# Optimization experiments

Measured on AMD Instinct MI355X. Metric: run time of the kernel, lower is better.

The kernel has to match this reference:

```python
import jax, jax.numpy as jnp
import numpy as np

B, N, C = 4, 4096, 64
K1, K2 = 4, 6
MLP1 = [128, 64, 64]
MLP2 = [128, 64]
EPS = 1e-5


def _sqdist(a, b):
    # a: [B,N,3], b: [B,M,3] -> [B,N,M]
    return (jnp.sum(a * a, -1)[:, :, None] + jnp.sum(b * b, -1)[:, None, :]
            - 2.0 * jnp.einsum('bnc,bmc->bnm', a, b))


def _knn_idx(k, xyz, new_xyz):
    # matches knn_point: topk of -square_distance(new_xyz, xyz)
    _, idx = jax.lax.top_k(-_sqdist(new_xyz, xyz), k)
    return idx  # [B,S,k]


def _gather(points, idx):
    # index_points: points [B,N,C], idx [B,S,K] -> [B,S,K,C]
    return jax.vmap(lambda p, i: p[i])(points, idx)


def _conv_bn_relu(x, w, g, b):
    # 1x1 Conv2d (no bias) + BatchNorm2d (train mode) + ReLU, channels-last
    y = jnp.einsum('bnkc,oc->bnko', x, w)
    m = jnp.mean(y, axis=(0, 1, 2), keepdims=True)
    v = jnp.var(y, axis=(0, 1, 2), keepdims=True)
    return jax.nn.relu((y - m) * jax.lax.rsqrt(v + EPS) * g + b)


def _quat_mul(a, b):
    # Hamilton product, matches mul_q_point ordering
    aw, ax, ay, az = a[..., 0], a[..., 1], a[..., 2], a[..., 3]
    bw, bx, by, bz = b[..., 0], b[..., 1], b[..., 2], b[..., 3]
    return jnp.stack([
        aw * bw - ax * bx - ay * by - az * bz,
        aw * bx + ax * bw + ay * bz - az * by,
        aw * by - ax * bz + ay * bw + az * bx,
        aw * bz + ax * by - ay * bx + az * bw], axis=-1)


def _inv_q(q):
    n2 = jnp.sum(q * q, -1, keepdims=True) + 1e-10
    return jnp.concatenate([q[..., :1], -q[..., 1:]], -1) / n2


def _qrot(q, v):
    # rotate points v [B,M,3] by quaternion q [B,4] via q * (0,v) * q^-1
    vq = jnp.concatenate([jnp.zeros(v.shape[:-1] + (1,), v.dtype), v], -1)
    qb = q[:, None, :]
    return _quat_mul(_quat_mul(qb, vq), _inv_q(q)[:, None, :])[..., 1:]


def setup_inputs() -> dict:
    key = jax.random.key(0)
    ks = jax.random.split(key, 32)

    def rn(i, shape, s=1.0):
        return jax.random.normal(ks[i], shape, jnp.float32) * s

    inp = {
        'pos1': rn(0, (B, N, 3)),
        'pos2': rn(1, (B, N, 3)),
        'feat1': rn(2, (B, N, C)),
        'feat2': rn(3, (B, N, C)),
        'q_coarse': rn(4, (B, 4)),
        't_coarse': rn(5, (B, 3)),
    }
    c1 = [2 * C + 3] + MLP1
    for i in range(len(MLP1)):
        inp['w1_%d' % i] = rn(6 + i, (c1[i + 1], c1[i]), 0.1)
        inp['g1_%d' % i] = jnp.ones((c1[i + 1],), jnp.float32)
        inp['b1_%d' % i] = jnp.zeros((c1[i + 1],), jnp.float32)
    c2 = [MLP1[-1] + C + 3] + MLP2
    for i in range(len(MLP2)):
        inp['w2_%d' % i] = rn(12 + i, (c2[i + 1], c2[i]), 0.1)
        inp['g2_%d' % i] = jnp.ones((c2[i + 1],), jnp.float32)
        inp['b2_%d' % i] = jnp.zeros((c2[i + 1],), jnp.float32)
    inp['wq'] = rn(20, (4, MLP2[-1]), 0.01)
    inp['bq'] = jnp.zeros((4,), jnp.float32)
    inp['wt'] = rn(21, (3, MLP2[-1]), 0.01)
    inp['bt'] = jnp.zeros((3,), jnp.float32)
    return inp


def reference(pos1, pos2, feat1, feat2, q_coarse, t_coarse,
              w1_0, g1_0, b1_0, w1_1, g1_1, b1_1, w1_2, g1_2, b1_2,
              w2_0, g2_0, b2_0, w2_1, g2_1, b2_1, wq, bq, wt, bt):
    # warp pos1 by the coarse pose (q, t)
    pos1_w = _qrot(q_coarse, pos1) + t_coarse[:, None, :]

    # cross-cloud KNN grouping (FlowEmbedding first stage)
    idx2 = _knn_idx(K2, pos2, pos1_w)                      # [B,N,K2]
    xd2 = _gather(pos2, idx2) - pos1_w[:, :, None, :]      # [B,N,K2,3]
    f2g = _gather(feat2, idx2)                             # [B,N,K2,C]
    f1r = jnp.broadcast_to(feat1[:, :, None, :], (B, N, K2, C))
    x = jnp.concatenate([xd2, f2g, f1r], -1)               # [B,N,K2,131]
    for w, g, b in ((w1_0, g1_0, b1_0), (w1_1, g1_1, b1_1), (w1_2, g1_2, b1_2)):
        x = _conv_bn_relu(x, w, g, b)
    fe = jnp.sum(x, axis=2)                                # [B,N,64] sum pool over neighbors

    # self KNN grouping (FlowEmbedding second stage)
    idx1 = _knn_idx(K1, pos1_w, pos1_w)                    # [B,N,K1]
    xd1 = _gather(pos1_w, idx1) - pos1_w[:, :, None, :]
    feg = _gather(fe, idx1)
    f1r2 = jnp.broadcast_to(feat1[:, :, None, :], (B, N, K1, C))
    x = jnp.concatenate([xd1, feg, f1r2], -1)              # [B,N,K1,131]
    for w, g, b in ((w2_0, g2_0, b2_0), (w2_1, g2_1, b2_1)):
        x = _conv_bn_relu(x, w, g, b)
    pooled = jnp.sum(jnp.sum(x, axis=2), axis=1)           # [B,64] sum pool

    # pose delta heads + quaternion composition
    q_det = pooled @ wq.T + bq
    q_det = q_det / (jnp.linalg.norm(q_det, axis=-1, keepdims=True) + 1e-10)
    t_det = pooled @ wt.T + bt
    q_new = _quat_mul(q_det, q_coarse)
    q_new = q_new / (jnp.linalg.norm(q_new, axis=-1, keepdims=True) + 1e-10)
    t_new = _qrot(q_det, t_coarse[:, None, :])[:, 0, :] + t_det
    return jnp.concatenate([q_new, t_new], -1)             # [B,7]
```

## Files before the change

kernel.cpp:

```cpp
#include <hip/hip_runtime.h>
#include <math.h>

#define B_ 4
#define N_ 4096
#define C_ 64
#define K1_ 4
#define K2_ 6
#define EPS_ 1e-5f
#define BN_ (B_ * N_)
#define NCH_ 16
#define CHP_ 256
#define STKD_ 16

typedef __attribute__((ext_vector_type(8))) short bf16x8;
typedef __attribute__((ext_vector_type(4))) float f32x4;
typedef __attribute__((ext_vector_type(2))) float f32x2;

__device__ __forceinline__ unsigned short f2bf(float f) {
  unsigned int u = __float_as_uint(f);
  unsigned int r = (u + 0x7fffu + ((u >> 16) & 1u)) >> 16;
  return (unsigned short)r;
}
__device__ __forceinline__ float bf2f(unsigned short u) {
  return __uint_as_float(((unsigned int)u) << 16);
}

__global__ __launch_bounds__(256) void k_init(
    const float* __restrict__ w1_0, const float* __restrict__ w1_1,
    const float* __restrict__ w1_2, const float* __restrict__ w2_0,
    const float* __restrict__ w2_1, unsigned short* __restrict__ Wf2a,
    unsigned short* __restrict__ Wf1a, unsigned short* __restrict__ Wfe,
    unsigned short* __restrict__ Wf1b, unsigned short* __restrict__ wb1,
    unsigned short* __restrict__ wb2, unsigned short* __restrict__ wb4,
    const float* __restrict__ pos1, const float* __restrict__ pos2,
    const float* __restrict__ qc, const float* __restrict__ tc,
    float* __restrict__ posw, float4* __restrict__ pts4w, float4* __restrict__ pairW,
    float4* __restrict__ pairP) {
  int t = blockIdx.x * 256 + threadIdx.x;
  int m = blockIdx.y;
  if (m < 7) {
    switch (m) {
      case 0:
        if (t < 8192) Wf2a[t] = f2bf(w1_0[(t >> 6) * 131 + 3 + (t & 63)]);
        break;
      case 1:
        if (t < 8192) Wf1a[t] = f2bf(w1_0[(t >> 6) * 131 + 67 + (t & 63)]);
        break;
      case 2:
        if (t < 8192) Wfe[t] = f2bf(w2_0[(t >> 6) * 131 + 3 + (t & 63)]);
        break;
      case 3:
        if (t < 8192) Wf1b[t] = f2bf(w2_0[(t >> 6) * 131 + 67 + (t & 63)]);
        break;
      case 4:
        if (t < 8192) wb1[t] = f2bf(w1_1[t]);
        break;
      case 5:
        if (t < 4096) wb2[t] = f2bf(w1_2[t]);
        break;
      default:
        if (t < 8192) wb4[t] = f2bf(w2_1[t]);
        break;
    }
    return;
  }
  if (t >= BN_) return;
  int b = t / N_;
  float qw = qc[b * 4 + 0], qx = qc[b * 4 + 1], qy = qc[b * 4 + 2], qz = qc[b * 4 + 3];
  float vx = pos1[t * 3 + 0], vy = pos1[t * 3 + 1], vz = pos1[t * 3 + 2];
  float aw = -(qx * vx + qy * vy + qz * vz);
  float ax = qw * vx + qy * vz - qz * vy;
  float ay = qw * vy - qx * vz + qz * vx;
  float az = qw * vz + qx * vy - qy * vx;
  float n2 = qw * qw + qx * qx + qy * qy + qz * qz + 1e-10f;
  float bw = qw / n2, bx = -qx / n2, by = -qy / n2, bz = -qz / n2;
  float rx = aw * bx + ax * bw + ay * bz - az * by;
  float ry = aw * by - ax * bz + ay * bw + az * bx;
  float rz = aw * bz + ax * by - ay * bx + az * bw;
  rx += tc[b * 3 + 0];
  ry += tc[b * 3 + 1];
  rz += tc[b * 3 + 2];
  posw[t * 3 + 0] = rx;
  posw[t * 3 + 1] = ry;
  posw[t * 3 + 2] = rz;
  float rw2 = rx * rx + ry * ry + rz * rz;
  pts4w[t] = make_float4(rx, ry, rz, rw2);
  int p = t >> 1, h = t & 1;
  float* bwp = (float*)&pairW[(size_t)2 * p];
  bwp[0 + h] = rx; bwp[2 + h] = ry; bwp[4 + h] = rz; bwp[6 + h] = rw2;
  float px = pos2[t * 3 + 0], py = pos2[t * 3 + 1], pz = pos2[t * 3 + 2];
  float pw2 = px * px + py * py + pz * pz;
  float* bpp = (float*)&pairP[(size_t)2 * p];
  bpp[0 + h] = px; bpp[2 + h] = py; bpp[4 + h] = pz; bpp[6 + h] = pw2;
}

__device__ __forceinline__ void ins6i(int (&kd)[6], int k) {
  int x = k;
#pragma unroll
  for (int u = 0; u < 6; ++u) {
    int lo = min(kd[u], x);
    x = max(kd[u], x);
    kd[u] = lo;
  }
}

__global__ __launch_bounds__(256) void k_knn2(const float4* __restrict__ pts4w,
                                              const float4* __restrict__ pairW,
                                              const float4* __restrict__ pairP,
                                              int* __restrict__ outK) {
  __shared__ int st[STKD_][256];
  int tid = threadIdx.x;
  int b = blockIdx.z & 3;
  int which = blockIdx.z >> 2;
  const f32x4* __restrict__ PT =
      (const f32x4*)((which ? pairW : pairP) + (size_t)b * N_ + blockIdx.y * CHP_);
  int base = blockIdx.y * CHP_;
  int n = blockIdx.x * 256 + tid;
  float4 qv = pts4w[(size_t)b * N_ + n];
  f32x2 qq2 = (f32x2)(qv.w);
  f32x2 m2x = (f32x2)(-2.f * qv.x);
  f32x2 m2y = (f32x2)(-2.f * qv.y);
  f32x2 m2z = (f32x2)(-2.f * qv.z);
  int kd[6];
#pragma unroll
  for (int t = 0; t < 6; ++t) kd[t] = 0x7fffffff;
  int kbd5 = 0x7fffffff;
  int ptr = 0;
  for (int jj = 0; jj < CHP_; jj += 4) {
    f32x4 e0 = PT[jj + 0];
    f32x4 e1 = PT[jj + 1];
    f32x4 e2 = PT[jj + 2];
    f32x4 e3 = PT[jj + 3];
    f32x2 d01 = __builtin_elementwise_fma(
        m2x, e0.xy,
        __builtin_elementwise_fma(m2y, e0.zw,
                                  __builtin_elementwise_fma(m2z, e1.xy, e1.zw + qq2)));
    f32x2 d23 = __builtin_elementwise_fma(
        m2x, e2.xy,
        __builtin_elementwise_fma(m2y, e2.zw,
                                  __builtin_elementwise_fma(m2z, e3.xy, e3.zw + qq2)));
    int j0 = base + jj;
    int k0 = (int)((__float_as_uint(d01.x) & 0xFFFFF000u) | (unsigned)(j0 + 0));
    int k1 = (int)((__float_as_uint(d01.y) & 0xFFFFF000u) | (unsigned)(j0 + 1));
    int k2 = (int)((__float_as_uint(d23.x) & 0xFFFFF000u) | (unsigned)(j0 + 2));
    int k3 = (int)((__float_as_uint(d23.y) & 0xFFFFF000u) | (unsigned)(j0 + 3));
    st[ptr][tid] = k0;
    ptr += (k0 < kbd5) ? 1 : 0;
    st[ptr][tid] = k1;
    ptr += (k1 < kbd5) ? 1 : 0;
    st[ptr][tid] = k2;
    ptr += (k2 < kbd5) ? 1 : 0;
    st[ptr][tid] = k3;
    ptr += (k3 < kbd5) ? 1 : 0;
    if (__ballot(ptr >= STKD_ - 4)) {
      for (int i = 0; i < ptr; ++i) ins6i(kd, st[i][tid]);
      ptr = 0;
      kbd5 = kd[5];
    }
  }
  for (int i = 0; i < ptr; ++i) ins6i(kd, st[i][tid]);
  size_t ob =
      ((size_t)which * BN_ * NCH_ + (size_t)(b * N_ + n) * NCH_ + blockIdx.y) * 6;
#pragma unroll
  for (int t = 0; t < 6; ++t) outK[ob + t] = kd[t];
}

__global__ __launch_bounds__(64) void k_knn2_merge(const int* __restrict__ inK,
                                                   int* __restrict__ idx2,
                                                   int* __restrict__ idx1) {
  int t = blockIdx.x * 64 + threadIdx.x;
  if (t >= 2 * BN_) return;
  int which = (t >= BN_) ? 1 : 0;
  int qi = t - which * BN_;
  int kd[6];
#pragma unroll
  for (int u = 0; u < 6; ++u) kd[u] = 0x7fffffff;
  size_t ib = ((size_t)which * BN_ + qi) * NCH_ * 6;
  for (int c = 0; c < NCH_ * 6; ++c) ins6i(kd, inK[ib + c]);
  if (which) {
#pragma unroll
    for (int u = 0; u < K1_; ++u) idx1[(size_t)qi * K1_ + u] = kd[u] & 0xFFF;
  } else {
#pragma unroll
    for (int u = 0; u < K2_; ++u) idx2[(size_t)qi * K2_ + u] = kd[u] & 0xFFF;
  }
}

__global__ __launch_bounds__(256) void k_proj(
    const float* __restrict__ s0, const unsigned short* __restrict__ w0,
    float* __restrict__ d0, const float* __restrict__ s1,
    const unsigned short* __restrict__ w1, float* __restrict__ d1,
    const float* __restrict__ s2, const unsigned short* __restrict__ w2,
    float* __restrict__ d2) {
  const float* src;
  const unsigned short* Wb;
  float* dst;
  switch (blockIdx.y) {
    case 0: src = s0; Wb = w0; dst = d0; break;
    case 1: src = s1; Wb = w1; dst = d1; break;
    default: src = s2; Wb = w2; dst = d2; break;
  }
  constexpr int SP = 72;
  __shared__ unsigned short Xs[64 * SP];
  int tid = threadIdx.x;
  int row0 = blockIdx.x * 64;
  for (int e = tid; e < 64 * 16; e += 256) {
    int r = e >> 4, s = e & 15;
    float4 v = *(const float4*)&src[(size_t)(row0 + r) * 64 + s * 4];
    ushort4 o;
    o.x = f2bf(v.x); o.y = f2bf(v.y); o.z = f2bf(v.z); o.w = f2bf(v.w);
    *(ushort4*)&Xs[r * SP + s * 4] = o;
  }
  __syncthreads();
  int l = tid & 63, wv = tid >> 6;
  int lm = l & 15, quad = l >> 4;
  int n0 = wv * 32;
  f32x4 acc[4][2];
#pragma unroll
  for (int rt = 0; rt < 4; ++rt)
#pragma unroll
    for (int ct = 0; ct < 2; ++ct) acc[rt][ct] = (f32x4)(0.f);
#pragma unroll
  for (int k0 = 0; k0 < 64; k0 += 32) {
    bf16x8 a[4], b[2];
#pragma unroll
    for (int rt = 0; rt < 4; ++rt)
      a[rt] = *(const bf16x8*)&Xs[(rt * 16 + lm) * SP + k0 + quad * 8];
#pragma unroll
    for (int ct = 0; ct < 2; ++ct)
      b[ct] = *(const bf16x8*)&Wb[(size_t)(n0 + ct * 16 + lm) * 64 + k0 + quad * 8];
#pragma unroll
    for (int rt = 0; rt < 4; ++rt)
#pragma unroll
      for (int ct = 0; ct < 2; ++ct)
        acc[rt][ct] =
            __builtin_amdgcn_mfma_f32_16x16x32_bf16(a[rt], b[ct], acc[rt][ct], 0, 0, 0);
  }
#pragma unroll
  for (int rt = 0; rt < 4; ++rt)
#pragma unroll
    for (int ct = 0; ct < 2; ++ct)
#pragma unroll
      for (int r = 0; r < 4; ++r) {
        int row = row0 + rt * 16 + quad * 4 + r;
        dst[(size_t)row * 128 + n0 + ct * 16 + lm] = acc[rt][ct][r];
      }
}

template <int KNN>
__global__ __launch_bounds__(256) void k_asm(
    const float* __restrict__ Wfull,
    const float* __restrict__ posP, const float* __restrict__ posw,
    const float* __restrict__ Pj, const float* __restrict__ Pn,
    const int* __restrict__ idx, unsigned short* __restrict__ yout,
    float* __restrict__ statOut) {
  __shared__ float Wx[3][128];
  __shared__ float red[16][128];
  int tid = threadIdx.x;
  if (tid < 128) {
    Wx[0][tid] = Wfull[tid * 131 + 0];
    Wx[1][tid] = Wfull[tid * 131 + 1];
    Wx[2][tid] = Wfull[tid * 131 + 2];
  }
  __syncthreads();
  int cg = tid & 15, rg = tid >> 4;
  int c0 = cg * 8;
  int row0 = blockIdx.x * 128 + rg * 8;
  float wx0[8], wx1[8], wx2[8];
#pragma unroll
  for (int u = 0; u < 8; ++u) {
    wx0[u] = Wx[0][c0 + u];
    wx1[u] = Wx[1][c0 + u];
    wx2[u] = Wx[2][c0 + u];
  }
  float s1[8], s2[8];
#pragma unroll
  for (int u = 0; u < 8; ++u) { s1[u] = 0.f; s2[u] = 0.f; }
#pragma unroll
  for (int i = 0; i < 8; ++i) {
    int row = row0 + i;
    int g = row / KNN;
    int bb = g >> 12;
    int j = idx[row];
    int gj = (bb << 12) + j;
    float xd0 = posP[(size_t)gj * 3 + 0] - posw[(size_t)g * 3 + 0];
    float xd1 = posP[(size_t)gj * 3 + 1] - posw[(size_t)g * 3 + 1];
    float xd2 = posP[(size_t)gj * 3 + 2] - posw[(size_t)g * 3 + 2];
    const float* pj = &Pj[(size_t)gj * 128 + c0];
    const float* pn = &Pn[(size_t)g * 128 + c0];
    float4 a0 = *(const float4*)&pj[0];
    float4 a1 = *(const float4*)&pj[4];
    float4 b0 = *(const float4*)&pn[0];
    float4 b1 = *(const float4*)&pn[4];
    float y[8];
    y[0] = a0.x + b0.x; y[1] = a0.y + b0.y; y[2] = a0.z + b0.z; y[3] = a0.w + b0.w;
    y[4] = a1.x + b1.x; y[5] = a1.y + b1.y; y[6] = a1.z + b1.z; y[7] = a1.w + b1.w;
    ushort4 o0, o1;
    unsigned short ob[8];
#pragma unroll
    for (int u = 0; u < 8; ++u) {
      float v = y[u];
      v = fmaf(xd0, wx0[u], v);
      v = fmaf(xd1, wx1[u], v);
      v = fmaf(xd2, wx2[u], v);
      s1[u] += v;
      s2[u] = fmaf(v, v, s2[u]);
      ob[u] = f2bf(v);
    }
    o0.x = ob[0]; o0.y = ob[1]; o0.z = ob[2]; o0.w = ob[3];
    o1.x = ob[4]; o1.y = ob[5]; o1.z = ob[6]; o1.w = ob[7];
    *(ushort4*)&yout[(size_t)row * 128 + c0] = o0;
    *(ushort4*)&yout[(size_t)row * 128 + c0 + 4] = o1;
  }
  int slot = blockIdx.x & 7;
#pragma unroll
  for (int u = 0; u < 8; ++u) red[rg][c0 + u] = s1[u];
  __syncthreads();
  if (tid < 128) {
    float s = 0.f;
#pragma unroll
    for (int r = 0; r < 16; ++r) s += red[r][tid];
    atomicAdd(&statOut[tid * 8 + slot], s);
  }
  __syncthreads();
#pragma unroll
  for (int u = 0; u < 8; ++u) red[rg][c0 + u] = s2[u];
  __syncthreads();
  if (tid < 128) {
    float s = 0.f;
#pragma unroll
    for (int r = 0; r < 16; ++r) s += red[r][tid];
    atomicAdd(&statOut[128 * 8 + tid * 8 + slot], s);
  }
}

template <int CIN, int COUT, int KP>
__global__ __launch_bounds__(256) void k_layer_mfma(
    const unsigned short* __restrict__ Wb,
    const unsigned short* __restrict__ yprev,
    const float* __restrict__ statPrev, const float* __restrict__ gPrev,
    const float* __restrict__ bPrev, float prevInvM,
    unsigned short* __restrict__ yout,
    float* __restrict__ statOut) {
  constexpr int SP = KP + 8;
  constexpr int CST = COUT + 8;
  constexpr int CT = COUT / 64;
  __shared__ unsigned short Xs[64 * SP];
  __shared__ float scl[CIN];
  __shared__ float shf[CIN];

  int tid = threadIdx.x;
  int row0 = blockIdx.x * 64;

  for (int c = tid; c < CIN; c += 256) {
    float s = 0.f, s2 = 0.f;
#pragma unroll
    for (int u = 0; u < 8; ++u) {
      s += statPrev[c * 8 + u];
      s2 += statPrev[CIN * 8 + c * 8 + u];
    }
    float m = s * prevInvM;
    float v = s2 * prevInvM - m * m;
    float sc = gPrev[c] * rsqrtf(v + EPS_);
    scl[c] = sc;
    shf[c] = bPrev[c] - m * sc;
  }
  __syncthreads();
  constexpr int S4 = KP / 4;
  for (int e = tid; e < 64 * S4; e += 256) {
    int r = e / S4, s = e - r * S4;
    int row = row0 + r;
    ushort4 u = *(const ushort4*)&yprev[(size_t)row * CIN + s * 4];
    ushort4 o;
    o.x = f2bf(fmaxf(fmaf(bf2f(u.x), scl[s * 4 + 0], shf[s * 4 + 0]), 0.f));
    o.y = f2bf(fmaxf(fmaf(bf2f(u.y), scl[s * 4 + 1], shf[s * 4 + 1]), 0.f));
    o.z = f2bf(fmaxf(fmaf(bf2f(u.z), scl[s * 4 + 2], shf[s * 4 + 2]), 0.f));
    o.w = f2bf(fmaxf(fmaf(bf2f(u.w), scl[s * 4 + 3], shf[s * 4 + 3]), 0.f));
    *(ushort4*)&Xs[r * SP + s * 4] = o;
  }
  __syncthreads();

  int l = tid & 63, wv = tid >> 6;
  int lm = l & 15, quad = l >> 4;
  int n0 = wv * (COUT / 4);

  f32x4 acc[4][CT];
#pragma unroll
  for (int rt = 0; rt < 4; ++rt)
#pragma unroll
    for (int ct = 0; ct < CT; ++ct) acc[rt][ct] = (f32x4)(0.f);

#pragma unroll
  for (int k0 = 0; k0 < KP; k0 += 32) {
    bf16x8 a[4], b[CT];
#pragma unroll
    for (int rt = 0; rt < 4; ++rt)
      a[rt] = *(const bf16x8*)&Xs[(rt * 16 + lm) * SP + k0 + quad * 8];
#pragma unroll
    for (int ct = 0; ct < CT; ++ct)
      b[ct] = *(const bf16x8*)&Wb[(size_t)(n0 + ct * 16 + lm) * KP + k0 + quad * 8];
#pragma unroll
    for (int rt = 0; rt < 4; ++rt)
#pragma unroll
      for (int ct = 0; ct < CT; ++ct)
        acc[rt][ct] =
            __builtin_amdgcn_mfma_f32_16x16x32_bf16(a[rt], b[ct], acc[rt][ct], 0, 0, 0);
  }

  int slot = blockIdx.x & 7;
#pragma unroll
  for (int ct = 0; ct < CT; ++ct) {
    float s1 = 0.f, s2 = 0.f;
#pragma unroll
    for (int rt = 0; rt < 4; ++rt)
#pragma unroll
      for (int r = 0; r < 4; ++r) {
        float v = acc[rt][ct][r];
        s1 += v;
        s2 += v * v;
      }
    s1 += __shfl_xor(s1, 16);
    s1 += __shfl_xor(s1, 32);
    s2 += __shfl_xor(s2, 16);
    s2 += __shfl_xor(s2, 32);
    if (quad == 0) {
      int col = n0 + ct * 16 + lm;
      atomicAdd(&statOut[col * 8 + slot], s1);
      atomicAdd(&statOut[COUT * 8 + col * 8 + slot], s2);
    }
  }

  __syncthreads();
  unsigned short* Ys = Xs;
#pragma unroll
  for (int rt = 0; rt < 4; ++rt)
#pragma unroll
    for (int ct = 0; ct < CT; ++ct)
#pragma unroll
      for (int r = 0; r < 4; ++r)
        Ys[(rt * 16 + quad * 4 + r) * CST + n0 + ct * 16 + lm] = f2bf(acc[rt][ct][r]);
  __syncthreads();
  constexpr int S8 = COUT / 8;
  for (int e = tid; e < 64 * S8; e += 256) {
    int r = e / S8, c0 = (e - r * S8) * 8;
    uint4 v = *(const uint4*)&Ys[r * CST + c0];
    *(uint4*)&yout[((size_t)(row0 + r)) * COUT + c0] = v;
  }
}

__global__ __launch_bounds__(256) void k_fe(const unsigned short* __restrict__ y3,
                                            const float* __restrict__ stat,
                                            const float* __restrict__ g,
                                            const float* __restrict__ bb,
                                            float* __restrict__ fe) {
  __shared__ float scl[C_], shf[C_];
  if (threadIdx.x < C_) {
    int c = threadIdx.x;
    float s = 0.f, s2 = 0.f;
#pragma unroll
    for (int u = 0; u < 8; ++u) {
      s += stat[c * 8 + u];
      s2 += stat[C_ * 8 + c * 8 + u];
    }
    const float invM = 1.f / (float)(BN_ * K2_);
    float m = s * invM;
    float v = s2 * invM - m * m;
    float sc = g[c] * rsqrtf(v + EPS_);
    scl[c] = sc;
    shf[c] = bb[c] - m * sc;
  }
  __syncthreads();
  int t = blockIdx.x * 256 + threadIdx.x;
  int bn = t >> 6, c = t & 63;
  float s = 0.f;
#pragma unroll
  for (int k = 0; k < K2_; ++k)
    s += fmaxf(fmaf(bf2f(y3[(size_t)(bn * K2_ + k) * C_ + c]), scl[c], shf[c]), 0.f);
  fe[t] = s;
}

__global__ __launch_bounds__(256) void k_pooled(const unsigned short* __restrict__ y5,
                                                const float* __restrict__ stat,
                                                const float* __restrict__ g,
                                                const float* __restrict__ bb,
                                                float* __restrict__ pooled) {
  __shared__ float scl[C_], shf[C_];
  __shared__ float red[4][C_];
  if (threadIdx.x < C_) {
    int c = threadIdx.x;
    float s = 0.f, s2 = 0.f;
#pragma unroll
    for (int u = 0; u < 8; ++u) {
      s += stat[c * 8 + u];
      s2 += stat[C_ * 8 + c * 8 + u];
    }
    const float invM = 1.f / (float)(BN_ * K1_);
    float m = s * invM;
    float v = s2 * invM - m * m;
    float sc = g[c] * rsqrtf(v + EPS_);
    scl[c] = sc;
    shf[c] = bb[c] - m * sc;
  }
  __syncthreads();
  int c = threadIdx.x & 63;
  int rs = threadIdx.x >> 6;
  int row0 = blockIdx.x * 64;
  int b = row0 / (N_ * K1_);
  float s = 0.f;
  for (int i = 0; i < 16; ++i) {
    int row = row0 + rs * 16 + i;
    s += fmaxf(fmaf(bf2f(y5[(size_t)row * C_ + c]), scl[c], shf[c]), 0.f);
  }
  red[rs][c] = s;
  __syncthreads();
  if (threadIdx.x < C_) {
    float t2 = red[0][c] + red[1][c] + red[2][c] + red[3][c];
    atomicAdd(&pooled[(b * C_ + c) * 8 + (blockIdx.x & 7)], t2);
  }
}

__global__ void k_final(const float* __restrict__ pooled, const float* __restrict__ wq,
                        const float* __restrict__ bq, const float* __restrict__ wt,
                        const float* __restrict__ bt, const float* __restrict__ qc,
                        const float* __restrict__ tc, float* __restrict__ out) {
  int b = threadIdx.x;
  if (b >= B_) return;
  float P[C_];
#pragma unroll
  for (int c = 0; c < C_; ++c) {
    float s = 0.f;
#pragma unroll
    for (int u = 0; u < 8; ++u) s += pooled[(b * C_ + c) * 8 + u];
    P[c] = s;
  }
  float qd[4];
#pragma unroll
  for (int i = 0; i < 4; ++i) {
    float s = bq[i];
#pragma unroll
    for (int c = 0; c < C_; ++c) s = fmaf(P[c], wq[i * C_ + c], s);
    qd[i] = s;
  }
  float td[3];
#pragma unroll
  for (int i = 0; i < 3; ++i) {
    float s = bt[i];
#pragma unroll
    for (int c = 0; c < C_; ++c) s = fmaf(P[c], wt[i * C_ + c], s);
    td[i] = s;
  }
  float nq = sqrtf(qd[0] * qd[0] + qd[1] * qd[1] + qd[2] * qd[2] + qd[3] * qd[3]) + 1e-10f;
#pragma unroll
  for (int i = 0; i < 4; ++i) qd[i] /= nq;
  float cw = qc[b * 4 + 0], cx = qc[b * 4 + 1], cyy = qc[b * 4 + 2], cz = qc[b * 4 + 3];
  float qnw = qd[0] * cw - qd[1] * cx - qd[2] * cyy - qd[3] * cz;
  float qnx = qd[0] * cx + qd[1] * cw + qd[2] * cz - qd[3] * cyy;
  float qny = qd[0] * cyy - qd[1] * cz + qd[2] * cw + qd[3] * cx;
  float qnz = qd[0] * cz + qd[1] * cyy - qd[2] * cx + qd[3] * cw;
  float nn = sqrtf(qnw * qnw + qnx * qnx + qny * qny + qnz * qnz) + 1e-10f;
  float vx = tc[b * 3 + 0], vy = tc[b * 3 + 1], vz = tc[b * 3 + 2];
  float aw = -(qd[1] * vx + qd[2] * vy + qd[3] * vz);
  float ax = qd[0] * vx + qd[2] * vz - qd[3] * vy;
  float ay = qd[0] * vy - qd[1] * vz + qd[3] * vx;
  float az = qd[0] * vz + qd[1] * vy - qd[2] * vx;
  float n2 = qd[0] * qd[0] + qd[1] * qd[1] + qd[2] * qd[2] + qd[3] * qd[3] + 1e-10f;
  float bw = qd[0] / n2, bx = -qd[1] / n2, by = -qd[2] / n2, bz = -qd[3] / n2;
  float rx = aw * bx + ax * bw + ay * bz - az * by;
  float ry = aw * by - ax * bz + ay * bw + az * bx;
  float rz = aw * bz + ax * by - ay * bx + az * bw;
  out[b * 7 + 0] = qnw / nn;
  out[b * 7 + 1] = qnx / nn;
  out[b * 7 + 2] = qny / nn;
  out[b * 7 + 3] = qnz / nn;
  out[b * 7 + 4] = rx + td[0];
  out[b * 7 + 5] = ry + td[1];
  out[b * 7 + 6] = rz + td[2];
}

extern "C" void kernel_launch(void* const* d_in, const int* in_sizes, int n_in,
                              void* d_out, int out_size, void* d_ws, size_t ws_size,
                              hipStream_t stream) {
  const float* pos1 = (const float*)d_in[0];
  const float* pos2 = (const float*)d_in[1];
  const float* feat1 = (const float*)d_in[2];
  const float* feat2 = (const float*)d_in[3];
  const float* qc = (const float*)d_in[4];
  const float* tc = (const float*)d_in[5];
  const float* w1_0 = (const float*)d_in[6];
  const float* g1_0 = (const float*)d_in[7];
  const float* b1_0 = (const float*)d_in[8];
  const float* w1_1 = (const float*)d_in[9];
  const float* g1_1 = (const float*)d_in[10];
  const float* b1_1 = (const float*)d_in[11];
  const float* w1_2 = (const float*)d_in[12];
  const float* g1_2 = (const float*)d_in[13];
  const float* b1_2 = (const float*)d_in[14];
  const float* w2_0 = (const float*)d_in[15];
  const float* g2_0 = (const float*)d_in[16];
  const float* b2_0 = (const float*)d_in[17];
  const float* w2_1 = (const float*)d_in[18];
  const float* g2_1 = (const float*)d_in[19];
  const float* b2_1 = (const float*)d_in[20];
  const float* wq = (const float*)d_in[21];
  const float* bq = (const float*)d_in[22];
  const float* wt = (const float*)d_in[23];
  const float* bt = (const float*)d_in[24];

  float* ws = (float*)d_ws;
  const size_t off_posw = 0;
  const size_t off_fe = 49152;
  const size_t off_stat = 1097728;
  const size_t off_pool = 1105920;
  const size_t off_idx2 = 1107968;
  const size_t off_idx1 = 1206272;
  const size_t off_wb = 1271808;
  const size_t off_pts4w = 1298432;
  const size_t off_pairW = 1363968;
  const size_t off_pairP = 1429504;
  const size_t off_P2a = 1495040;
  const size_t off_P1a = 3592192;
  const size_t off_P1b = 5689344;
  const size_t off_Pfe = 7786496;
  const size_t off_yA = 9883648;
  const size_t off_yB = 16175104;

  float* posw = ws + off_posw;
  float* fe = ws + off_fe;
  float* stat0 = ws + off_stat;
  float* stat1 = stat0 + 2048;
  float* stat2 = stat1 + 1024;
  float* stat3 = stat2 + 1024;
  float* stat4 = stat3 + 2048;
  float* pooled = ws + off_pool;
  int* idx2 = (int*)(ws + off_idx2);
  int* idx1 = (int*)(ws + off_idx1);
  unsigned short* Wf2a = (unsigned short*)(ws + off_wb);
  unsigned short* Wf1a = Wf2a + 8192;
  unsigned short* Wfe = Wf1a + 8192;
  unsigned short* Wf1b = Wfe + 8192;
  unsigned short* wb1 = Wf1b + 8192;
  unsigned short* wb2 = wb1 + 8192;
  unsigned short* wb4 = wb2 + 4096;
  float4* pts4w = (float4*)(ws + off_pts4w);
  float4* pairW = (float4*)(ws + off_pairW);
  float4* pairP = (float4*)(ws + off_pairP);
  float* P2a = ws + off_P2a;
  float* P1a = ws + off_P1a;
  float* P1b = ws + off_P1b;
  float* Pfe = ws + off_Pfe;
  unsigned short* yA = (unsigned short*)(ws + off_yA);
  unsigned short* yB = (unsigned short*)(ws + off_yB);
  int* knnK = (int*)yA;

  hipMemsetAsync(ws + off_stat, 0, (8192 + 2048) * sizeof(float), stream);

  k_init<<<dim3(64, 8), 256, 0, stream>>>(w1_0, w1_1, w1_2, w2_0, w2_1, Wf2a, Wf1a,
                                          Wfe, Wf1b, wb1, wb2, wb4, pos1, pos2, qc, tc,
                                          posw, pts4w, pairW, pairP);

  k_knn2<<<dim3(N_ / 256, NCH_, 2 * B_), 256, 0, stream>>>(pts4w, pairW, pairP, knnK);
  k_knn2_merge<<<dim3(2 * BN_ / 64), 64, 0, stream>>>(knnK, idx2, idx1);

  k_proj<<<dim3(256, 3), 256, 0, stream>>>(feat2, Wf2a, P2a, feat1, Wf1a, P1a, feat1,
                                           Wf1b, P1b);
  k_asm<K2_><<<dim3(98304 / 128), 256, 0, stream>>>(w1_0, pos2, posw, P2a, P1a, idx2,
                                                    yA, stat0);
  k_layer_mfma<128, 64, 128><<<dim3(1536), 256, 0, stream>>>(
      wb1, yA, stat0, g1_0, b1_0, 1.f / 98304.f, yB, stat1);
  k_layer_mfma<64, 64, 64><<<dim3(1536), 256, 0, stream>>>(
      wb2, yB, stat1, g1_1, b1_1, 1.f / 98304.f, yA, stat2);
  k_fe<<<dim3(BN_ * C_ / 256), 256, 0, stream>>>(yA, stat2, g1_2, b1_2, fe);
  k_proj<<<dim3(256, 1), 256, 0, stream>>>(fe, Wfe, Pfe, nullptr, nullptr, nullptr,
                                           nullptr, nullptr, nullptr);
  k_asm<K1_><<<dim3(65536 / 128), 256, 0, stream>>>(w2_0, posw, posw, Pfe, P1b, idx1,
                                                    yA, stat3);
  k_layer_mfma<128, 64, 128><<<dim3(1024), 256, 0, stream>>>(
      wb4, yA, stat3, g2_0, b2_0, 1.f / 65536.f, yB, stat4);
  k_pooled<<<dim3(65536 / 64), 256, 0, stream>>>(yB, stat4, g2_1, b2_1, pooled);
  k_final<<<dim3(1), 64, 0, stream>>>(pooled, wq, bq, wt, bt, qc, tc, (float*)d_out);
}
```

Before: 386.8 us.

## Fuse fe pooling into projection; restructure MFMA layer to row-per-wave with register weights

Merges the BN+ReLU+neighbor-sum kernel for fe with the following bf16 projection, so fe no longer goes through an fp32 global buffer and one launch disappears. The MFMA layer kernel now gives each wave 16 rows and all output columns, keeping the full weight tile in registers. BN statistics are reduced in shared memory before a single atomic per column, which cuts global atomics. Holding more weights in registers per wave may raise register pressure.

```diff
diff --git a/kernel.cpp b/kernel.cpp
--- a/kernel.cpp
+++ b/kernel.cpp
@@ -186,6 +186,46 @@
   }
 }
 
+__device__ __forceinline__ void proj_mfma_tail(const unsigned short* Xs, int tid,
+                                               int row0,
+                                               const unsigned short* __restrict__ Wb,
+                                               float* __restrict__ dst) {
+  constexpr int SP = 72;
+  int l = tid & 63, wv = tid >> 6;
+  int lm = l & 15, quad = l >> 4;
+  int n0 = wv * 32;
+  f32x4 acc[4][2];
+#pragma unroll
+  for (int rt = 0; rt < 4; ++rt)
+#pragma unroll
+    for (int ct = 0; ct < 2; ++ct) acc[rt][ct] = (f32x4)(0.f);
+#pragma unroll
+  for (int k0 = 0; k0 < 64; k0 += 32) {
+    bf16x8 a[4], b[2];
+#pragma unroll
+    for (int rt = 0; rt < 4; ++rt)
+      a[rt] = *(const bf16x8*)&Xs[(rt * 16 + lm) * SP + k0 + quad * 8];
+#pragma unroll
+    for (int ct = 0; ct < 2; ++ct)
+      b[ct] = *(const bf16x8*)&Wb[(size_t)(n0 + ct * 16 + lm) * 64 + k0 + quad * 8];
+#pragma unroll
+    for (int rt = 0; rt < 4; ++rt)
+#pragma unroll
+      for (int ct = 0; ct < 2; ++ct)
+        acc[rt][ct] =
+            __builtin_amdgcn_mfma_f32_16x16x32_bf16(a[rt], b[ct], acc[rt][ct], 0, 0, 0);
+  }
+#pragma unroll
+  for (int rt = 0; rt < 4; ++rt)
+#pragma unroll
+    for (int ct = 0; ct < 2; ++ct)
+#pragma unroll
+      for (int r = 0; r < 4; ++r) {
+        int row = row0 + rt * 16 + quad * 4 + r;
+        dst[(size_t)row * 128 + n0 + ct * 16 + lm] = acc[rt][ct][r];
+      }
+}
+
 __global__ __launch_bounds__(256) void k_proj(
     const float* __restrict__ s0, const unsigned short* __restrict__ w0,
     float* __restrict__ d0, const float* __restrict__ s1,
@@ -212,39 +252,54 @@
     *(ushort4*)&Xs[r * SP + s * 4] = o;
   }
   __syncthreads();
-  int l = tid & 63, wv = tid >> 6;
-  int lm = l & 15, quad = l >> 4;
-  int n0 = wv * 32;
-  f32x4 acc[4][2];
-#pragma unroll
-  for (int rt = 0; rt < 4; ++rt)
-#pragma unroll
-    for (int ct = 0; ct < 2; ++ct) acc[rt][ct] = (f32x4)(0.f);
-#pragma unroll
-  for (int k0 = 0; k0 < 64; k0 += 32) {
-    bf16x8 a[4], b[2];
-#pragma unroll
-    for (int rt = 0; rt < 4; ++rt)
-      a[rt] = *(const bf16x8*)&Xs[(rt * 16 + lm) * SP + k0 + quad * 8];
-#pragma unroll
-    for (int ct = 0; ct < 2; ++ct)
-      b[ct] = *(const bf16x8*)&Wb[(size_t)(n0 + ct * 16 + lm) * 64 + k0 + quad * 8];
-#pragma unroll
-    for (int rt = 0; rt < 4; ++rt)
-#pragma unroll
-      for (int ct = 0; ct < 2; ++ct)
-        acc[rt][ct] =
-            __builtin_amdgcn_mfma_f32_16x16x32_bf16(a[rt], b[ct], acc[rt][ct], 0, 0, 0);
-  }
-#pragma unroll
-  for (int rt = 0; rt < 4; ++rt)
-#pragma unroll
-    for (int ct = 0; ct < 2; ++ct)
-#pragma unroll
-      for (int r = 0; r < 4; ++r) {
-        int row = row0 + rt * 16 + quad * 4 + r;
-        dst[(size_t)row * 128 + n0 + ct * 16 + lm] = acc[rt][ct][r];
-      }
+  proj_mfma_tail(Xs, tid, row0, Wb, dst);
+}
+
+__global__ __launch_bounds__(256) void k_feproj(const unsigned short* __restrict__ y3,
+                                                const float* __restrict__ stat,
+                                                const float* __restrict__ g,
+                                                const float* __restrict__ bb,
+                                                const unsigned short* __restrict__ Wfe,
+                                                float* __restrict__ Pfe) {
+  constexpr int SP = 72;
+  __shared__ unsigned short Xs[64 * SP];
+  __shared__ float scl[C_], shf[C_];
+  int tid = threadIdx.x;
+  if (tid < C_) {
+    int c = tid;
+    float s = 0.f, s2 = 0.f;
+#pragma unroll
+    for (int u = 0; u < 8; ++u) {
+      s += stat[c * 8 + u];
+      s2 += stat[C_ * 8 + c * 8 + u];
+    }
+    const float invM = 1.f / (float)(BN_ * K2_);
+    float m = s * invM;
+    float v = s2 * invM - m * m;
+    float sc = g[c] * rsqrtf(v + EPS_);
+    scl[c] = sc;
+    shf[c] = bb[c] - m * sc;
+  }
+  __syncthreads();
+  int row0 = blockIdx.x * 64;
+  for (int e = tid; e < 64 * 16; e += 256) {
+    int r = e >> 4, s = e & 15;
+    size_t base = ((size_t)(row0 + r) * K2_) * C_ + s * 4;
+    float a0 = 0.f, a1 = 0.f, a2 = 0.f, a3 = 0.f;
+#pragma unroll
+    for (int k = 0; k < K2_; ++k) {
+      ushort4 u = *(const ushort4*)&y3[base + (size_t)k * C_];
+      a0 += fmaxf(fmaf(bf2f(u.x), scl[s * 4 + 0], shf[s * 4 + 0]), 0.f);
+      a1 += fmaxf(fmaf(bf2f(u.y), scl[s * 4 + 1], shf[s * 4 + 1]), 0.f);
+      a2 += fmaxf(fmaf(bf2f(u.z), scl[s * 4 + 2], shf[s * 4 + 2]), 0.f);
+      a3 += fmaxf(fmaf(bf2f(u.w), scl[s * 4 + 3], shf[s * 4 + 3]), 0.f);
+    }
+    ushort4 o;
+    o.x = f2bf(a0); o.y = f2bf(a1); o.z = f2bf(a2); o.w = f2bf(a3);
+    *(ushort4*)&Xs[r * SP + s * 4] = o;
+  }
+  __syncthreads();
+  proj_mfma_tail(Xs, tid, row0, Wfe, Pfe);
 }
 
 template <int KNN>
@@ -344,10 +399,12 @@
     float* __restrict__ statOut) {
   constexpr int SP = KP + 8;
   constexpr int CST = COUT + 8;
-  constexpr int CT = COUT / 64;
+  constexpr int CT = COUT / 16;
+  constexpr int NK = KP / 32;
   __shared__ unsigned short Xs[64 * SP];
   __shared__ float scl[CIN];
   __shared__ float shf[CIN];
+  __shared__ float redS[8][COUT];
 
   int tid = threadIdx.x;
   int row0 = blockIdx.x * 64;
@@ -382,63 +439,65 @@
 
   int l = tid & 63, wv = tid >> 6;
   int lm = l & 15, quad = l >> 4;
-  int n0 = wv * (COUT / 4);
-
-  f32x4 acc[4][CT];
-#pragma unroll
-  for (int rt = 0; rt < 4; ++rt)
-#pragma unroll
-    for (int ct = 0; ct < CT; ++ct) acc[rt][ct] = (f32x4)(0.f);
-
-#pragma unroll
-  for (int k0 = 0; k0 < KP; k0 += 32) {
-    bf16x8 a[4], b[CT];
-#pragma unroll
-    for (int rt = 0; rt < 4; ++rt)
-      a[rt] = *(const bf16x8*)&Xs[(rt * 16 + lm) * SP + k0 + quad * 8];
+
+  const unsigned short* wbase = &Wb[(size_t)lm * KP + quad * 8];
+  const unsigned short* arow = &Xs[(wv * 16 + lm) * SP + quad * 8];
+
+  bf16x8 Breg[NK][CT];
+#pragma unroll
+  for (int kk = 0; kk < NK; ++kk)
 #pragma unroll
     for (int ct = 0; ct < CT; ++ct)
-      b[ct] = *(const bf16x8*)&Wb[(size_t)(n0 + ct * 16 + lm) * KP + k0 + quad * 8];
-#pragma unroll
-    for (int rt = 0; rt < 4; ++rt)
-#pragma unroll
-      for (int ct = 0; ct < CT; ++ct)
-        acc[rt][ct] =
-            __builtin_amdgcn_mfma_f32_16x16x32_bf16(a[rt], b[ct], acc[rt][ct], 0, 0, 0);
-  }
-
-  int slot = blockIdx.x & 7;
+      Breg[kk][ct] = *(const bf16x8*)&wbase[(size_t)ct * 16 * KP + kk * 32];
+
+  f32x4 acc[CT];
+#pragma unroll
+  for (int ct = 0; ct < CT; ++ct) acc[ct] = (f32x4)(0.f);
+#pragma unroll
+  for (int kk = 0; kk < NK; ++kk) {
+    bf16x8 a = *(const bf16x8*)&arow[kk * 32];
+#pragma unroll
+    for (int ct = 0; ct < CT; ++ct)
+      acc[ct] = __builtin_amdgcn_mfma_f32_16x16x32_bf16(a, Breg[kk][ct], acc[ct], 0, 0, 0);
+  }
+
 #pragma unroll
   for (int ct = 0; ct < CT; ++ct) {
     float s1 = 0.f, s2 = 0.f;
 #pragma unroll
-    for (int rt = 0; rt < 4; ++rt)
-#pragma unroll
-      for (int r = 0; r < 4; ++r) {
-        float v = acc[rt][ct][r];
-        s1 += v;
-        s2 += v * v;
-      }
+    for (int r = 0; r < 4; ++r) {
+      float v = acc[ct][r];
+      s1 += v;
+      s2 += v * v;
+    }
     s1 += __shfl_xor(s1, 16);
     s1 += __shfl_xor(s1, 32);
     s2 += __shfl_xor(s2, 16);
     s2 += __shfl_xor(s2, 32);
     if (quad == 0) {
-      int col = n0 + ct * 16 + lm;
-      atomicAdd(&statOut[col * 8 + slot], s1);
-      atomicAdd(&statOut[COUT * 8 + col * 8 + slot], s2);
-    }
+      int col = ct * 16 + lm;
+      redS[wv][col] = s1;
+      redS[4 + wv][col] = s2;
+    }
+  }
+  __syncthreads();
+  int slot = blockIdx.x & 7;
+  if (tid < COUT) {
+    float s = redS[0][tid] + redS[1][tid] + redS[2][tid] + redS[3][tid];
+    atomicAdd(&statOut[tid * 8 + slot], s);
+  } else if (tid < 2 * COUT) {
+    int c = tid - COUT;
+    float s = redS[4][c] + redS[5][c] + redS[6][c] + redS[7][c];
+    atomicAdd(&statOut[COUT * 8 + c * 8 + slot], s);
   }
 
   __syncthreads();
   unsigned short* Ys = Xs;
 #pragma unroll
-  for (int rt = 0; rt < 4; ++rt)
-#pragma unroll
-    for (int ct = 0; ct < CT; ++ct)
-#pragma unroll
-      for (int r = 0; r < 4; ++r)
-        Ys[(rt * 16 + quad * 4 + r) * CST + n0 + ct * 16 + lm] = f2bf(acc[rt][ct][r]);
+  for (int ct = 0; ct < CT; ++ct)
+#pragma unroll
+    for (int r = 0; r < 4; ++r)
+      Ys[(wv * 16 + quad * 4 + r) * CST + ct * 16 + lm] = f2bf(acc[ct][r]);
   __syncthreads();
   constexpr int S8 = COUT / 8;
   for (int e = tid; e < 64 * S8; e += 256) {
@@ -446,37 +505,6 @@
     uint4 v = *(const uint4*)&Ys[r * CST + c0];
     *(uint4*)&yout[((size_t)(row0 + r)) * COUT + c0] = v;
   }
-}
-
-__global__ __launch_bounds__(256) void k_fe(const unsigned short* __restrict__ y3,
-                                            const float* __restrict__ stat,
-                                            const float* __restrict__ g,
-                                            const float* __restrict__ bb,
-                                            float* __restrict__ fe) {
-  __shared__ float scl[C_], shf[C_];
-  if (threadIdx.x < C_) {
-    int c = threadIdx.x;
-    float s = 0.f, s2 = 0.f;
-#pragma unroll
-    for (int u = 0; u < 8; ++u) {
-      s += stat[c * 8 + u];
-      s2 += stat[C_ * 8 + c * 8 + u];
-    }
-    const float invM = 1.f / (float)(BN_ * K2_);
-    float m = s * invM;
-    float v = s2 * invM - m * m;
-    float sc = g[c] * rsqrtf(v + EPS_);
-    scl[c] = sc;
-    shf[c] = bb[c] - m * sc;
-  }
-  __syncthreads();
-  int t = blockIdx.x * 256 + threadIdx.x;
-  int bn = t >> 6, c = t & 63;
-  float s = 0.f;
-#pragma unroll
-  for (int k = 0; k < K2_; ++k)
-    s += fmaxf(fmaf(bf2f(y3[(size_t)(bn * K2_ + k) * C_ + c]), scl[c], shf[c]), 0.f);
-  fe[t] = s;
 }
 
 __global__ __launch_bounds__(256) void k_pooled(const unsigned short* __restrict__ y5,
@@ -608,24 +636,22 @@
 
   float* ws = (float*)d_ws;
   const size_t off_posw = 0;
-  const size_t off_fe = 49152;
-  const size_t off_stat = 1097728;
-  const size_t off_pool = 1105920;
-  const size_t off_idx2 = 1107968;
-  const size_t off_idx1 = 1206272;
-  const size_t off_wb = 1271808;
-  const size_t off_pts4w = 1298432;
-  const size_t off_pairW = 1363968;
-  const size_t off_pairP = 1429504;
-  const size_t off_P2a = 1495040;
-  const size_t off_P1a = 3592192;
-  const size_t off_P1b = 5689344;
-  const size_t off_Pfe = 7786496;
-  const size_t off_yA = 9883648;
-  const size_t off_yB = 16175104;
+  const size_t off_stat = 49152;
+  const size_t off_pool = 57344;
+  const size_t off_idx2 = 59392;
+  const size_t off_idx1 = 157696;
+  const size_t off_wb = 223232;
+  const size_t off_pts4w = 249856;
+  const size_t off_pairW = 315392;
+  const size_t off_pairP = 380928;
+  const size_t off_P2a = 446464;
+  const size_t off_P1a = 2543616;
+  const size_t off_P1b = 4640768;
+  const size_t off_Pfe = 6737920;
+  const size_t off_yA = 8835072;
+  const size_t off_yB = 15126528;
 
   float* posw = ws + off_posw;
-  float* fe = ws + off_fe;
   float* stat0 = ws + off_stat;
   float* stat1 = stat0 + 2048;
   float* stat2 = stat1 + 1024;
@@ -669,9 +695,7 @@
       wb1, yA, stat0, g1_0, b1_0, 1.f / 98304.f, yB, stat1);
   k_layer_mfma<64, 64, 64><<<dim3(1536), 256, 0, stream>>>(
       wb2, yB, stat1, g1_1, b1_1, 1.f / 98304.f, yA, stat2);
-  k_fe<<<dim3(BN_ * C_ / 256), 256, 0, stream>>>(yA, stat2, g1_2, b1_2, fe);
-  k_proj<<<dim3(256, 1), 256, 0, stream>>>(fe, Wfe, Pfe, nullptr, nullptr, nullptr,
-                                           nullptr, nullptr, nullptr);
+  k_feproj<<<dim3(256), 256, 0, stream>>>(yA, stat2, g1_2, b1_2, Wfe, Pfe);
   k_asm<K1_><<<dim3(65536 / 128), 256, 0, stream>>>(w2_0, posw, posw, Pfe, P1b, idx1,
                                                     yA, stat3);
   k_layer_mfma<128, 64, 128><<<dim3(1024), 256, 0, stream>>>(
```

After: 390.4 us. Within noise of the previous version (+0.9%).
